# Performance work log

Hardware: AMD Instinct MI355X
Metric: run time of the kernel (lower is better)

Reference implementation:

```python
import jax, jax.numpy as jnp
import numpy as np

G, N, E = 4, 50000, 400000   # subgraphs, nodes/graph, edges/graph
D = 128                      # num_node_feat = num_g_hid = out_g_ch
L = 3                        # num_layers
NE, AH = 8, 64               # num_expert, num_att_hid
FE = 8                       # num_edge_feat (unused by GIN conv)
LN_EPS = 1e-5


def setup_inputs() -> dict:
    key = jax.random.key(0)
    ks = jax.random.split(key, 12)
    s = 1.0 / np.sqrt(D)
    inp = {
        "decomp_x": jax.random.normal(ks[0], (G, N, D), dtype=jnp.float32),
        "decomp_edge_index": jax.random.randint(ks[1], (G, 2, E), 0, N, dtype=jnp.int32),
        "decomp_edge_attr": jax.random.normal(ks[2], (G, E, FE), dtype=jnp.float32),
        # GIN MLP params per layer: Linear(D,D) -> ReLU -> Linear(D,D), stored [in,out]
        "Ws1": jax.random.uniform(ks[3], (L, D, D), jnp.float32, -s, s),
        "bs1": jax.random.uniform(ks[4], (L, D), jnp.float32, -s, s),
        "Ws2": jax.random.uniform(ks[5], (L, D, D), jnp.float32, -s, s),
        "bs2": jax.random.uniform(ks[6], (L, D), jnp.float32, -s, s),
        "ln_g": jnp.ones((L, D), jnp.float32),
        "ln_b": jnp.zeros((L, D), jnp.float32),
        # Attention: w1 [n_hidden, v_hidden], w2 [n_expert, n_hidden]
        "att_w1": jax.random.uniform(ks[7], (AH, D), jnp.float32, -1.0 / np.sqrt(D), 1.0 / np.sqrt(D)),
        "att_w2": jax.random.uniform(ks[8], (NE, AH), jnp.float32, -1.0 / np.sqrt(AH), 1.0 / np.sqrt(AH)),
    }
    return inp


def _layer_norm(h, g, b):
    mu = jnp.mean(h, axis=-1, keepdims=True)
    var = jnp.var(h, axis=-1, keepdims=True)
    return (h - mu) * jax.lax.rsqrt(var + LN_EPS) * g + b


def _gin_graph(x, edge_index, Ws1, bs1, Ws2, bs2, ln_g, ln_b):
    # x: [N, D]; edge_index: [2, E] (src, dst)
    src, dst = edge_index[0], edge_index[1]
    for l in range(L):
        identity = x
        # GINConv (eps=0): MLP(x_i + sum_{j->i} x_j)
        agg = jax.ops.segment_sum(x[src], dst, num_segments=N)  # gather+scatter
        h = x + agg
        h = jnp.maximum(h @ Ws1[l] + bs1[l], 0.0) @ Ws2[l] + bs2[l]
        if l < L - 1:
            h = h + identity  # same dims, no projection
        x = _layer_norm(h, ln_g[l], ln_b[l])
    return jnp.sum(x, axis=0)  # [D] graph readout (sum over nodes)


def reference(decomp_x, decomp_edge_index, decomp_edge_attr,
              Ws1, bs1, Ws2, bs2, ln_g, ln_b, att_w1, att_w2):
    # edge_attr is unused by the GIN conv path (only NaN-checked in torch)
    g = jax.vmap(_gin_graph, in_axes=(0, 0, None, None, None, None, None, None))(
        decomp_x, decomp_edge_index, Ws1, bs1, Ws2, bs2, ln_g, ln_b)  # [G, D]
    # Attention pooling over subgraph vectors
    support = jnp.tanh(att_w1 @ g.T)                 # [AH, G]
    att = jax.nn.softmax(att_w2 @ support, axis=1)   # [NE, G]
    pooled = att @ g                                 # [NE, D]
    return pooled.reshape(1, NE * D)                 # [1, NE*D]
```

## Files before the change

kernel.cpp:

```cpp
#include <hip/hip_runtime.h>
#include <math.h>

#define G 4
#define NN 50000
#define EE 400000
#define D 128
#define LN_EPS 1e-5f
#define BPG 782
#define SM 50008
#define CH 2048
#define NCH ((NN + CH - 1) / CH)

typedef _Float16 f16;
typedef _Float16 f16x4 __attribute__((ext_vector_type(4)));
typedef _Float16 f16x8 __attribute__((ext_vector_type(8)));
typedef float f32x4 __attribute__((ext_vector_type(4)));


__global__ __launch_bounds__(256) void hist_kernel(const int* __restrict__ ei, int* __restrict__ deg) {
    int idx = blockIdx.x * 256 + threadIdx.x;
    if (idx >= G * EE) return;
    int g = idx / EE, e = idx - g * EE;
    int dst = ei[g * 2 * EE + EE + e];
    atomicAdd(&deg[g * NN + dst], 1);
}


__global__ __launch_bounds__(256) void scan_part(const int* __restrict__ deg, int* __restrict__ E,
                                                 int* __restrict__ part) {
    int b = blockIdx.x;
    int g = b / NCH, c = b - g * NCH;
    int t = threadIdx.x;
    int base = c * CH + t * 8;
    const int* dg = deg + g * NN;
    int v[8];
    int s = 0;
#pragma unroll
    for (int j = 0; j < 8; ++j) {
        int i = base + j;
        v[j] = (i < NN) ? dg[i] : 0;
        s += v[j];
    }
    __shared__ int sums[256];
    sums[t] = s;
    __syncthreads();
    for (int off = 1; off < 256; off <<= 1) {
        int x = (t >= off) ? sums[t - off] : 0;
        __syncthreads();
        sums[t] += x;
        __syncthreads();
    }
    int run = (t == 0) ? 0 : sums[t - 1];
    int* Eg = E + g * SM;
#pragma unroll
    for (int j = 0; j < 8; ++j) {
        int i = base + j;
        if (i < NN) Eg[1 + i] = run;
        run += v[j];
    }
    if (t == 255) part[g * NCH + c] = sums[255];
    if (c == 0 && t == 0) Eg[0] = 0;
}

__global__ __launch_bounds__(128) void scan_tops(int* __restrict__ part) {
    int g = blockIdx.x, t = threadIdx.x;
    __shared__ int s[128];
    int v = (t < NCH) ? part[g * NCH + t] : 0;
    s[t] = v;
    __syncthreads();
    for (int off = 1; off < 128; off <<= 1) {
        int x = (t >= off) ? s[t - off] : 0;
        __syncthreads();
        s[t] += x;
        __syncthreads();
    }
    if (t < NCH) part[g * NCH + t] = s[t] - v;
}

__global__ __launch_bounds__(256) void scan_add(const int* __restrict__ part, int* __restrict__ E) {
    int b = blockIdx.x;
    int g = b / NCH, c = b - g * NCH;
    int off = part[g * NCH + c];
    if (off == 0) return;
    int t = threadIdx.x;
    int base = c * CH + t * 8;
    int* Eg = E + g * SM + 1;
#pragma unroll
    for (int j = 0; j < 8; ++j) {
        int i = base + j;
        if (i < NN) Eg[i] += off;
    }
}

__global__ __launch_bounds__(256) void place_kernel(const int* __restrict__ ei, int* __restrict__ E,
                                                    int* __restrict__ csr_src) {
    int idx = blockIdx.x * 256 + threadIdx.x;
    if (idx >= G * EE) return;
    int g = idx / EE, e = idx - g * EE;
    int src = ei[g * 2 * EE + e];
    int dst = ei[g * 2 * EE + EE + e];
    int pos = atomicAdd(&E[g * SM + 1 + dst], 1);
    csr_src[g * EE + pos] = src;
}


__global__ __launch_bounds__(256) void cast_x_kernel(const float* __restrict__ x, f16* __restrict__ o) {
    int i = blockIdx.x * 256 + threadIdx.x;
    float4 v = ((const float4*)x)[i];
    f16x4 h = {(f16)v.x, (f16)v.y, (f16)v.z, (f16)v.w};
    ((f16x4*)o)[i] = h;
}

__global__ __launch_bounds__(256) void cast_w_kernel(const float* __restrict__ Ws1, const float* __restrict__ Ws2,
                                                     f16* __restrict__ Wt) {
    int e = blockIdx.x * 256 + threadIdx.x;
    int mat = e >> 14, r = (e >> 7) & 127, c = e & 127;
    const float* src = (mat < 3) ? (Ws1 + mat * 16384) : (Ws2 + (mat - 3) * 16384);
    Wt[e] = (f16)src[c * 128 + r];
}


__global__ __launch_bounds__(256, 8) void gin_layer(
    const f16* __restrict__ Xin, f16* __restrict__ Xout,
    const int* __restrict__ E, const int* __restrict__ csr_src,
    const f16* __restrict__ W1t, const f16* __restrict__ W2t,
    const float* __restrict__ b1, const float* __restrict__ b2,
    const float* __restrict__ lng, const float* __restrict__ lnb,
    int has_res, int do_read, float* __restrict__ gvec)
{
    __shared__ f16 A[64][136];
    __shared__ float colsum[128];

    int t = threadIdx.x;
    int slot = blockIdx.x & 7;
    int gi = blockIdx.x >> 3;
    int g = slot & 3;
    int bb = (slot >> 2) * 391 + gi;
    int nrow0 = bb * 64;
    long row0 = (long)g * NN + nrow0;
    int valid = min(64, NN - nrow0);

    if (do_read) {
        if (t < 128) colsum[t] = 0.f;
        __syncthreads();
    }

    {
        int grp = t >> 4, lane = t & 15;
        const int* rs = E + g * SM;
        const int* srcs = csr_src + (long)g * EE;
        long gbase = (long)g * NN * 16;
        const f16x8* Xv = (const f16x8*)Xin;
#pragma unroll
        for (int i = 0; i < 4; ++i) {
            int r = grp * 4 + i;
            if (r < valid) {
                int n = nrow0 + r;
                f16x8 self = Xv[(row0 + r) * 16 + lane];
                float acc[8];
#pragma unroll
                for (int j = 0; j < 8; ++j) acc[j] = (float)self[j];
                int s0 = rs[n], s1 = rs[n + 1];
                int k = s0;
                for (; k + 1 < s1; k += 2) {
                    f16x8 v0 = Xv[gbase + (long)srcs[k] * 16 + lane];
                    f16x8 v1 = Xv[gbase + (long)srcs[k + 1] * 16 + lane];
#pragma unroll
                    for (int j = 0; j < 8; ++j) acc[j] += (float)v0[j] + (float)v1[j];
                }
                if (k < s1) {
                    f16x8 v0 = Xv[gbase + (long)srcs[k] * 16 + lane];
#pragma unroll
                    for (int j = 0; j < 8; ++j) acc[j] += (float)v0[j];
                }
                f16x8 o;
#pragma unroll
                for (int j = 0; j < 8; ++j) o[j] = (f16)acc[j];
                *(f16x8*)&A[r][lane * 8] = o;
            } else {
                f16x8 z = {0, 0, 0, 0, 0, 0, 0, 0};
                *(f16x8*)&A[r][lane * 8] = z;
            }
        }
    }

    int w = t >> 6, l = t & 63, q = l >> 4, cl = l & 15;
    int mrow = w * 16 + cl;

    const f16x8* Wb1 = (const f16x8*)W1t + (cl * 16 + q);
    f32x4 acc[8];
#pragma unroll
    for (int ns = 0; ns < 8; ++ns) acc[ns] = (f32x4){0.f, 0.f, 0.f, 0.f};
#pragma unroll
    for (int kc = 0; kc < 4; ++kc) {
        f16x8 a = *(const f16x8*)&A[mrow][kc * 32 + q * 8];
#pragma unroll
        for (int ns = 0; ns < 8; ++ns) {
            f16x8 b = Wb1[ns * 256 + kc * 4];
            acc[ns] = __builtin_amdgcn_mfma_f32_16x16x32_f16(a, b, acc[ns], 0, 0, 0);
        }
    }

#pragma unroll
    for (int ns = 0; ns < 8; ++ns) {
        float bv = b1[ns * 16 + cl];
#pragma unroll
        for (int r = 0; r < 4; ++r) {
            float v = fmaxf(acc[ns][r] + bv, 0.f);
            A[w * 16 + q * 4 + r][ns * 16 + cl] = (f16)v;
        }
    }

    const f16x8* Wb2 = (const f16x8*)W2t + (cl * 16 + q);
    f32x4 acc2[8];
#pragma unroll
    for (int ns = 0; ns < 8; ++ns) acc2[ns] = (f32x4){0.f, 0.f, 0.f, 0.f};
#pragma unroll
    for (int kc = 0; kc < 4; ++kc) {
        f16x8 a = *(const f16x8*)&A[mrow][kc * 32 + q * 8];
#pragma unroll
        for (int ns = 0; ns < 8; ++ns) {
            f16x8 b = Wb2[ns * 256 + kc * 4];
            acc2[ns] = __builtin_amdgcn_mfma_f32_16x16x32_f16(a, b, acc2[ns], 0, 0, 0);
        }
    }

    float o[8][4];
    float gm[8], gb[8];
#pragma unroll
    for (int ns = 0; ns < 8; ++ns) {
        int col = ns * 16 + cl;
        float b2v = b2[col];
        gm[ns] = lng[col];
        gb[ns] = lnb[col];
#pragma unroll
        for (int r = 0; r < 4; ++r) o[ns][r] = acc2[ns][r] + b2v;
    }
    if (has_res) {
#pragma unroll
        for (int r = 0; r < 4; ++r) {
            int lr = w * 16 + q * 4 + r;
            if (lr < valid) {
                const f16* xr = Xin + (row0 + lr) * 128 + cl;
#pragma unroll
                for (int ns = 0; ns < 8; ++ns) o[ns][r] += (float)xr[ns * 16];
            }
        }
    }

#pragma unroll
    for (int r = 0; r < 4; ++r) {
        float s1 = 0.f, s2 = 0.f;
#pragma unroll
        for (int ns = 0; ns < 8; ++ns) { s1 += o[ns][r]; s2 += o[ns][r] * o[ns][r]; }
        s1 += __shfl_xor(s1, 1); s2 += __shfl_xor(s2, 1);
        s1 += __shfl_xor(s1, 2); s2 += __shfl_xor(s2, 2);
        s1 += __shfl_xor(s1, 4); s2 += __shfl_xor(s2, 4);
        s1 += __shfl_xor(s1, 8); s2 += __shfl_xor(s2, 8);
        float mean = s1 * (1.f / 128.f);
        float var = s2 * (1.f / 128.f) - mean * mean;
        float rstd = rsqrtf(var + LN_EPS);
#pragma unroll
        for (int ns = 0; ns < 8; ++ns) o[ns][r] = (o[ns][r] - mean) * rstd * gm[ns] + gb[ns];
    }

    if (!do_read) {
#pragma unroll
        for (int ns = 0; ns < 8; ++ns)
#pragma unroll
            for (int r = 0; r < 4; ++r)
                A[w * 16 + q * 4 + r][ns * 16 + cl] = (f16)o[ns][r];
        int rr = w * 16 + (l >> 2), seg = l & 3;
        if (rr < valid) {
            f16* dst = Xout + (row0 + rr) * 128 + seg * 32;
            const f16* srcp = &A[rr][seg * 32];
            *(f16x8*)(dst)      = *(const f16x8*)(srcp);
            *(f16x8*)(dst + 8)  = *(const f16x8*)(srcp + 8);
            *(f16x8*)(dst + 16) = *(const f16x8*)(srcp + 16);
            *(f16x8*)(dst + 24) = *(const f16x8*)(srcp + 24);
        }
    } else {
#pragma unroll
        for (int ns = 0; ns < 8; ++ns) {
            float v = 0.f;
#pragma unroll
            for (int r = 0; r < 4; ++r) {
                int lr = w * 16 + q * 4 + r;
                if (lr < valid) v += o[ns][r];
            }
            v += __shfl_xor(v, 16);
            v += __shfl_xor(v, 32);
            if (l < 16) atomicAdd(&colsum[ns * 16 + cl], v);
        }
        __syncthreads();
        if (t < 128) atomicAdd(&gvec[g * 128 + t], colsum[t]);
    }
}


__global__ __launch_bounds__(256) void att_kernel(const float* __restrict__ gvec, const float* __restrict__ w1,
                                                  const float* __restrict__ w2, float* __restrict__ out) {
    __shared__ float sup[64][4];
    __shared__ float att[8][4];
    int t = threadIdx.x;
    int ah = t >> 2, gg = t & 3;
    float d = 0.f;
    for (int k = 0; k < 128; ++k) d += w1[ah * 128 + k] * gvec[gg * 128 + k];
    sup[ah][gg] = tanhf(d);
    __syncthreads();
    if (t < 32) {
        int ne = t >> 2, g2 = t & 3;
        float sc = 0.f;
        for (int k = 0; k < 64; ++k) sc += w2[ne * 64 + k] * sup[k][g2];
        att[ne][g2] = sc;
    }
    __syncthreads();
    if (t < 8) {
        float m = fmaxf(fmaxf(att[t][0], att[t][1]), fmaxf(att[t][2], att[t][3]));
        float e0 = expf(att[t][0] - m), e1 = expf(att[t][1] - m);
        float e2 = expf(att[t][2] - m), e3 = expf(att[t][3] - m);
        float inv = 1.f / (e0 + e1 + e2 + e3);
        att[t][0] = e0 * inv; att[t][1] = e1 * inv; att[t][2] = e2 * inv; att[t][3] = e3 * inv;
    }
    __syncthreads();
    for (int o = t; o < 1024; o += 256) {
        int ne = o >> 7, dd = o & 127;
        float v = 0.f;
        for (int g2 = 0; g2 < 4; ++g2) v += att[ne][g2] * gvec[g2 * 128 + dd];
        out[o] = v;
    }
}


extern "C" void kernel_launch(void* const* d_in, const int* in_sizes, int n_in,
                              void* d_out, int out_size, void* d_ws, size_t ws_size,
                              hipStream_t stream) {
    const float* x   = (const float*)d_in[0];
    const int*   ei  = (const int*)d_in[1];
    const float* Ws1 = (const float*)d_in[3];
    const float* bs1 = (const float*)d_in[4];
    const float* Ws2 = (const float*)d_in[5];
    const float* bs2 = (const float*)d_in[6];
    const float* lng = (const float*)d_in[7];
    const float* lnb = (const float*)d_in[8];
    const float* aw1 = (const float*)d_in[9];
    const float* aw2 = (const float*)d_in[10];

    char* ws = (char*)d_ws;
    f16*   XA       = (f16*)(ws);
    f16*   XB       = (f16*)(ws + 51200000);
    int*   csr_src  = (int*)(ws + 102400000);
    int*   E        = (int*)(ws + 108800000);
    f16*   Wt       = (f16*)(ws + 109600256);
    float* gvec     = (float*)(ws + 109796864);
    int*   part     = (int*)(ws + 109798912);
    int*   deg      = (int*)(ws + 51200000);

    hipMemsetAsync(deg, 0, G * NN * sizeof(int), stream);
    hipMemsetAsync(gvec, 0, G * D * sizeof(float), stream);

    hist_kernel<<<(G * EE + 255) / 256, 256, 0, stream>>>(ei, deg);
    scan_part<<<G * NCH, 256, 0, stream>>>(deg, E, part);
    scan_tops<<<G, 128, 0, stream>>>(part);
    scan_add<<<G * NCH, 256, 0, stream>>>(part, E);
    place_kernel<<<(G * EE + 255) / 256, 256, 0, stream>>>(ei, E, csr_src);

    cast_x_kernel<<<(G * NN * D / 4) / 256, 256, 0, stream>>>(x, XA);
    cast_w_kernel<<<(6 * D * D) / 256, 256, 0, stream>>>(Ws1, Ws2, Wt);

    f16* Xcur = XA;
    f16* Xnxt = XB;
    for (int l = 0; l < 3; ++l) {
        gin_layer<<<G * BPG, 256, 0, stream>>>(Xcur, Xnxt, E, csr_src,
                                               Wt + l * D * D, Wt + (3 + l) * D * D,
                                               bs1 + l * D, bs2 + l * D,
                                               lng + l * D, lnb + l * D,
                                               (l < 2) ? 1 : 0, (l == 2) ? 1 : 0, gvec);
        f16* tmp = Xcur; Xcur = Xnxt; Xnxt = tmp;
    }
    att_kernel<<<1, 256, 0, stream>>>(gvec, aw1, aw2, (float*)d_out);
}
```

Baseline: 911.8 us.

## Merge prep kernels, fold scan tops into add, cache residual rows in LDS

Combines the x cast, weight cast, degree histogram and gvec zeroing into one launch, and merges the scan-tops pass into the scan-add kernel so each block sums the chunk partials itself. The GIN layer now keeps each node's own features in a second shared tile during aggregation and reads the residual from there, instead of reading them again from global memory. The extra LDS tile means the occupancy hint is lowered from 8 to 4 blocks per CU. The residual loop no longer checks for padding rows, but for layers that add the residual those rows are never written to memory, so it is harmless.

```diff
diff --git a/kernel.cpp b/kernel.cpp
--- a/kernel.cpp
+++ b/kernel.cpp
@@ -11,18 +11,44 @@
 #define CH 2048
 #define NCH ((NN + CH - 1) / CH)
 
+#define FB_CASTX 25000
+#define FB_CASTW (FB_CASTX + 384)
+#define FB_HIST  (FB_CASTW + 6250)
+#define FB_TOTAL (FB_HIST + 1)
+
 typedef _Float16 f16;
 typedef _Float16 f16x4 __attribute__((ext_vector_type(4)));
 typedef _Float16 f16x8 __attribute__((ext_vector_type(8)));
 typedef float f32x4 __attribute__((ext_vector_type(4)));
 
 
-__global__ __launch_bounds__(256) void hist_kernel(const int* __restrict__ ei, int* __restrict__ deg) {
-    int idx = blockIdx.x * 256 + threadIdx.x;
-    if (idx >= G * EE) return;
-    int g = idx / EE, e = idx - g * EE;
-    int dst = ei[g * 2 * EE + EE + e];
-    atomicAdd(&deg[g * NN + dst], 1);
+__global__ __launch_bounds__(256) void prep_fat(const float* __restrict__ x,
+                                                const float* __restrict__ Ws1, const float* __restrict__ Ws2,
+                                                const int* __restrict__ ei,
+                                                f16* __restrict__ XA, f16* __restrict__ Wt,
+                                                int* __restrict__ deg, float* __restrict__ gvec) {
+    int b = blockIdx.x, t = threadIdx.x;
+    if (b < FB_CASTX) {
+        int i = b * 256 + t;
+        float4 v = ((const float4*)x)[i];
+        f16x4 h = {(f16)v.x, (f16)v.y, (f16)v.z, (f16)v.w};
+        ((f16x4*)XA)[i] = h;
+    } else if (b < FB_CASTW) {
+        int e = (b - FB_CASTX) * 256 + t;
+        int mat = e >> 14, r = (e >> 7) & 127, c = e & 127;
+        const float* src = (mat < 3) ? (Ws1 + mat * 16384) : (Ws2 + (mat - 3) * 16384);
+        Wt[e] = (f16)src[c * 128 + r];
+    } else if (b < FB_HIST) {
+        int idx = (b - FB_CASTW) * 256 + t;
+        if (idx < G * EE) {
+            int g = idx / EE, e = idx - g * EE;
+            int dst = ei[g * 2 * EE + EE + e];
+            atomicAdd(&deg[g * NN + dst], 1);
+        }
+    } else {
+        gvec[t] = 0.f;
+        gvec[256 + t] = 0.f;
+    }
 }
 
 
@@ -62,27 +88,16 @@
     if (c == 0 && t == 0) Eg[0] = 0;
 }
 
-__global__ __launch_bounds__(128) void scan_tops(int* __restrict__ part) {
-    int g = blockIdx.x, t = threadIdx.x;
-    __shared__ int s[128];
-    int v = (t < NCH) ? part[g * NCH + t] : 0;
-    s[t] = v;
-    __syncthreads();
-    for (int off = 1; off < 128; off <<= 1) {
-        int x = (t >= off) ? s[t - off] : 0;
-        __syncthreads();
-        s[t] += x;
-        __syncthreads();
-    }
-    if (t < NCH) part[g * NCH + t] = s[t] - v;
-}
-
-__global__ __launch_bounds__(256) void scan_add(const int* __restrict__ part, int* __restrict__ E) {
+__global__ __launch_bounds__(256) void scan_addtops(const int* __restrict__ part, int* __restrict__ E) {
     int b = blockIdx.x;
     int g = b / NCH, c = b - g * NCH;
-    int off = part[g * NCH + c];
+    int t = threadIdx.x;
+    __shared__ int sp[NCH];
+    if (t < NCH) sp[t] = part[g * NCH + t];
+    __syncthreads();
+    int off = 0;
+    for (int j = 0; j < c; ++j) off += sp[j];
     if (off == 0) return;
-    int t = threadIdx.x;
     int base = c * CH + t * 8;
     int* Eg = E + g * SM + 1;
 #pragma unroll
@@ -104,23 +119,7 @@
 }
 
 
-__global__ __launch_bounds__(256) void cast_x_kernel(const float* __restrict__ x, f16* __restrict__ o) {
-    int i = blockIdx.x * 256 + threadIdx.x;
-    float4 v = ((const float4*)x)[i];
-    f16x4 h = {(f16)v.x, (f16)v.y, (f16)v.z, (f16)v.w};
-    ((f16x4*)o)[i] = h;
-}
-
-__global__ __launch_bounds__(256) void cast_w_kernel(const float* __restrict__ Ws1, const float* __restrict__ Ws2,
-                                                     f16* __restrict__ Wt) {
-    int e = blockIdx.x * 256 + threadIdx.x;
-    int mat = e >> 14, r = (e >> 7) & 127, c = e & 127;
-    const float* src = (mat < 3) ? (Ws1 + mat * 16384) : (Ws2 + (mat - 3) * 16384);
-    Wt[e] = (f16)src[c * 128 + r];
-}
-
-
-__global__ __launch_bounds__(256, 8) void gin_layer(
+__global__ __launch_bounds__(256, 4) void gin_layer(
     const f16* __restrict__ Xin, f16* __restrict__ Xout,
     const int* __restrict__ E, const int* __restrict__ csr_src,
     const f16* __restrict__ W1t, const f16* __restrict__ W2t,
@@ -129,6 +128,7 @@
     int has_res, int do_read, float* __restrict__ gvec)
 {
     __shared__ f16 A[64][136];
+    __shared__ f16 ID[64][136];
     __shared__ float colsum[128];
 
     int t = threadIdx.x;
@@ -157,6 +157,7 @@
             if (r < valid) {
                 int n = nrow0 + r;
                 f16x8 self = Xv[(row0 + r) * 16 + lane];
+                if (has_res) *(f16x8*)&ID[r][lane * 8] = self;
                 float acc[8];
 #pragma unroll
                 for (int j = 0; j < 8; ++j) acc[j] = (float)self[j];
@@ -240,11 +241,8 @@
 #pragma unroll
         for (int r = 0; r < 4; ++r) {
             int lr = w * 16 + q * 4 + r;
-            if (lr < valid) {
-                const f16* xr = Xin + (row0 + lr) * 128 + cl;
-#pragma unroll
-                for (int ns = 0; ns < 8; ++ns) o[ns][r] += (float)xr[ns * 16];
-            }
+#pragma unroll
+            for (int ns = 0; ns < 8; ++ns) o[ns][r] += (float)ID[lr][ns * 16 + cl];
         }
     }
 
@@ -357,16 +355,12 @@
     int*   deg      = (int*)(ws + 51200000);
 
     hipMemsetAsync(deg, 0, G * NN * sizeof(int), stream);
-    hipMemsetAsync(gvec, 0, G * D * sizeof(float), stream);
-
-    hist_kernel<<<(G * EE + 255) / 256, 256, 0, stream>>>(ei, deg);
+
+    prep_fat<<<FB_TOTAL, 256, 0, stream>>>(x, Ws1, Ws2, ei, XA, Wt, deg, gvec);
+
     scan_part<<<G * NCH, 256, 0, stream>>>(deg, E, part);
-    scan_tops<<<G, 128, 0, stream>>>(part);
-    scan_add<<<G * NCH, 256, 0, stream>>>(part, E);
+    scan_addtops<<<G * NCH, 256, 0, stream>>>(part, E);
     place_kernel<<<(G * EE + 255) / 256, 256, 0, stream>>>(ei, E, csr_src);
-
-    cast_x_kernel<<<(G * NN * D / 4) / 256, 256, 0, stream>>>(x, XA);
-    cast_w_kernel<<<(6 * D * D) / 256, 256, 0, stream>>>(Ws1, Ws2, Wt);
 
     f16* Xcur = XA;
     f16* Xnxt = XB;
```

Measured after the change: 867.4 us. 1.05x faster.
